# Kernel optimization log

Hardware: AMD Instinct MI355X
Metric: run time of the kernel (lower is better)

## Reference

```python
import jax, jax.numpy as jnp
import numpy as np

N_NODES = 100000
N_EDGES = 1600000
DIM = 128
N_LAYERS = 3
N_GRAPHS = 2048


def setup_inputs() -> dict:
    key = jax.random.key(0)
    ks = jax.random.split(key, 6)
    x = jax.random.normal(ks[0], (N_NODES, DIM), dtype=jnp.float32)
    edge_index = jax.random.randint(ks[1], (2, N_EDGES), 0, N_NODES, dtype=jnp.int64)
    batch = jnp.sort(jax.random.randint(ks[2], (N_NODES,), 0, N_GRAPHS, dtype=jnp.int64))
    scale = 1.0 / np.sqrt(DIM)
    W1 = jax.random.normal(ks[3], (N_LAYERS, DIM, DIM), dtype=jnp.float32) * scale
    b1 = jnp.zeros((N_LAYERS, DIM), dtype=jnp.float32)
    W2 = jax.random.normal(ks[4], (N_LAYERS, DIM, DIM), dtype=jnp.float32) * scale
    b2 = jnp.zeros((N_LAYERS, DIM), dtype=jnp.float32)
    return {"x": x, "edge_index": edge_index, "batch": batch,
            "W1": W1, "b1": b1, "W2": W2, "b2": b2}


def reference(x, edge_index, batch, W1, b1, W2, b2):
    src, dst = edge_index[0], edge_index[1]
    n = x.shape[0]
    n_layers = W1.shape[0]
    for l in range(n_layers):
        # GINConv (eps=0): h_i = MLP( sum_{j in N(i)} x_j + x_i )
        agg = jax.ops.segment_sum(x[src], dst, num_segments=n)  # [N, D]
        h = agg + x
        h = jnp.maximum(h @ W1[l] + b1[l], 0.0) @ W2[l] + b2[l]
        x = jnp.maximum(h, 0.0)  # outer self.act
    # global_mean_pool over graph ids
    sums = jax.ops.segment_sum(x, batch, num_segments=N_GRAPHS)  # [G, D]
    counts = jax.ops.segment_sum(jnp.ones((n,), x.dtype), batch, num_segments=N_GRAPHS)
    return sums / jnp.maximum(counts, 1.0)[:, None]
```

## Files before the change

### kernel.cpp

```cpp
#include <hip/hip_runtime.h>
#include <hip/hip_bf16.h>
#include <stdint.h>

#define N_NODES  100000
#define N_PAD    100032
#define N_EDGES  1600000
#define DIM      128
#define N_LAYERS 3
#define N_GRAPHS 2048

#define BSHIFT   8
#define NBUCKET  391
#define P1CHUNK  4096
#define P1GRID   391

typedef _Float16 f16;
typedef __attribute__((ext_vector_type(4))) _Float16 f16x4;
typedef __attribute__((ext_vector_type(8))) _Float16 f16x8;
typedef __attribute__((ext_vector_type(4))) float f32x4;

#define MFMA16(a, b, c) __builtin_amdgcn_mfma_f32_16x16x32_f16((a), (b), (c), 0, 0, 0)

#define OFF_OFFS  0u
#define OFF_BHT   400064u
#define OFF_BST   401664u
#define OFF_GCUR  403264u
#define OFF_BLKH  404864u
#define OFF_ESRC  1016448u
#define OFF_PAIR  7416448u
#define OFF_X16   13816448u
#define OFF_A16   39424640u
#define OFF_B16   65032832u
#define OFF_W1T   90641024u
#define OFF_W2T   90739328u


__global__ __launch_bounds__(256) void k_bhist(const int* __restrict__ dst,
                                               int* __restrict__ btot, int* __restrict__ blkh) {
    __shared__ int h[NBUCKET];
    int tid = threadIdx.x, b = blockIdx.x;
    for (int i = tid; i < NBUCKET; i += 256) h[i] = 0;
    __syncthreads();
    int base = b * P1CHUNK;
    int n = min(P1CHUNK, N_EDGES - base);
    for (int i = tid; i < n; i += 256)
        atomicAdd(&h[dst[base + i] >> BSHIFT], 1);
    __syncthreads();
    for (int i = tid; i < NBUCKET; i += 256) {
        blkh[b * NBUCKET + i] = h[i];
        atomicAdd(&btot[i], h[i]);
    }
}

__global__ __launch_bounds__(256) void k_bscan(const int* __restrict__ btot,
                                               int* __restrict__ bstart,
                                               int* __restrict__ gcursor,
                                               int* __restrict__ offs) {
    __shared__ int s[512];
    int t = threadIdx.x;
    s[t]       = (t < NBUCKET) ? btot[t] : 0;
    s[t + 256] = (t + 256 < NBUCKET) ? btot[t + 256] : 0;
    __syncthreads();
    for (int off = 1; off < 512; off <<= 1) {
        int a0 = (t >= off) ? s[t - off] : 0;
        int a1 = (t + 256 >= off) ? s[t + 256 - off] : 0;
        __syncthreads();
        s[t] += a0; s[t + 256] += a1;
        __syncthreads();
    }
    int e0 = (t == 0) ? 0 : s[t - 1];
    int e1 = s[t + 255];
    if (t < NBUCKET) { bstart[t] = e0; gcursor[t] = e0; }
    int idx = t + 256;
    if (idx <= NBUCKET) { bstart[idx] = e1; if (idx < NBUCKET) gcursor[idx] = e1; }
    if (t == 0) offs[N_NODES] = N_EDGES;
}

__global__ __launch_bounds__(256) void k_part1(const int* __restrict__ src, const int* __restrict__ dst,
                                               const int* __restrict__ blkh, int* __restrict__ gcursor,
                                               uint32_t* __restrict__ pairs) {
    __shared__ int gbase[NBUCKET];
    __shared__ int cur[NBUCKET];
    int tid = threadIdx.x, b = blockIdx.x;
    for (int i = tid; i < NBUCKET; i += 256) {
        int h = blkh[b * NBUCKET + i];
        gbase[i] = atomicAdd(&gcursor[i], h);
        cur[i] = 0;
    }
    __syncthreads();
    int base = b * P1CHUNK;
    int n = min(P1CHUNK, N_EDGES - base);
    for (int i = tid; i < n; i += 256) {
        int d = dst[base + i], s = src[base + i];
        int bin = d >> BSHIFT;
        int slot = atomicAdd(&cur[bin], 1);
        pairs[gbase[bin] + slot] = ((uint32_t)s << 8) | (uint32_t)(d & 255);
    }
}

__global__ __launch_bounds__(256) void k_part2(const uint32_t* __restrict__ pairs,
                                               const int* __restrict__ bstart,
                                               int* __restrict__ offs, int* __restrict__ esrc) {
    __shared__ int cnt[256];
    __shared__ int cur[256];
    __shared__ int sc[256];
    int t = threadIdx.x, b = blockIdx.x;
    int n0 = b << BSHIFT;
    int nn = min(256, N_NODES - n0);
    int e0 = bstart[b], e1 = bstart[b + 1];
    cnt[t] = 0;
    __syncthreads();
    for (int i = e0 + t; i < e1; i += 256)
        atomicAdd(&cnt[pairs[i] & 255], 1);
    __syncthreads();
    int my = cnt[t];
    sc[t] = my;
    __syncthreads();
    for (int off = 1; off < 256; off <<= 1) {
        int v = (t >= off) ? sc[t - off] : 0;
        __syncthreads();
        sc[t] += v;
        __syncthreads();
    }
    int excl = sc[t] - my;
    cur[t] = excl;
    if (t < nn) offs[n0 + t] = e0 + excl;
    __syncthreads();
    for (int i = e0 + t; i < e1; i += 256) {
        uint32_t p = pairs[i];
        int pos = e0 + atomicAdd(&cur[p & 255], 1);
        esrc[pos] = (int)(p >> 8);
    }
}


__global__ void k_cvtX(const float* __restrict__ x, f16* __restrict__ o) {
    size_t i = ((size_t)blockIdx.x * 256 + threadIdx.x) * 8;
    float4 v0 = *(const float4*)&x[i];
    float4 v1 = *(const float4*)&x[i + 4];
    f16x8 h;
    h[0] = (f16)v0.x; h[1] = (f16)v0.y; h[2] = (f16)v0.z; h[3] = (f16)v0.w;
    h[4] = (f16)v1.x; h[5] = (f16)v1.y; h[6] = (f16)v1.z; h[7] = (f16)v1.w;
    *(f16x8*)&o[i] = h;
}

__global__ void k_cvtW(const float* __restrict__ W1, const float* __restrict__ W2,
                       f16* __restrict__ W1t, f16* __restrict__ W2t) {
    int t = blockIdx.x * 256 + threadIdx.x;
    bool first = t < 49152;
    const float* W = first ? W1 : W2;
    f16* Wt = first ? W1t : W2t;
    int u = first ? t : t - 49152;
    int l = u >> 14;
    int kn = u & 16383;
    int k = kn >> 7, nn = kn & 127;
    Wt[l * 16384 + nn * 128 + k] = (f16)W[u];
}


#define BM 64
#define LDS_K 136

__global__ __launch_bounds__(256) void k_fused(
    const f16* __restrict__ xin, f16* __restrict__ xout,
    const int* __restrict__ offs, const int* __restrict__ esrc,
    const f16* __restrict__ W1t, const float* __restrict__ b1,
    const f16* __restrict__ W2t, const float* __restrict__ b2)
{
    __shared__ __align__(16) f16 tile[BM * LDS_K];
    int tid  = threadIdx.x;
    int lane = tid & 63;
    int w    = tid >> 6;
    int fr   = lane & 15;
    int fg   = lane >> 4;
    int row0 = blockIdx.x * BM;

    {
        const f16x8* xr = (const f16x8*)xin;
        int c = fr;
#pragma unroll
        for (int t4 = 0; t4 < 4; t4++) {
            int r = w * 16 + t4 * 4 + fg;
            int node = row0 + r;
            f16x8 sum = {(f16)0, (f16)0, (f16)0, (f16)0, (f16)0, (f16)0, (f16)0, (f16)0};
            if (node < N_NODES) {
                sum = xr[(size_t)node * 16 + c];
                int e0 = offs[node], e1 = offs[node + 1];
                int e = e0;
                for (; e + 8 <= e1; e += 8) {
                    int s0 = esrc[e + 0], s1 = esrc[e + 1], s2 = esrc[e + 2], s3 = esrc[e + 3];
                    int s4 = esrc[e + 4], s5 = esrc[e + 5], s6 = esrc[e + 6], s7 = esrc[e + 7];
                    f16x8 v0 = xr[(size_t)s0 * 16 + c], v1 = xr[(size_t)s1 * 16 + c];
                    f16x8 v2 = xr[(size_t)s2 * 16 + c], v3 = xr[(size_t)s3 * 16 + c];
                    f16x8 v4 = xr[(size_t)s4 * 16 + c], v5 = xr[(size_t)s5 * 16 + c];
                    f16x8 v6 = xr[(size_t)s6 * 16 + c], v7 = xr[(size_t)s7 * 16 + c];
                    sum += (v0 + v1) + (v2 + v3);
                    sum += (v4 + v5) + (v6 + v7);
                }
                if (e < e1) {
                    int i1 = e + 1, i2 = e + 2, i3 = e + 3, i4 = e + 4, i5 = e + 5, i6 = e + 6, i7 = e + 7;
                    bool k1 = i1 < e1, k2 = i2 < e1, k3 = i3 < e1, k4 = i4 < e1,
                         k5 = i5 < e1, k6 = i6 < e1, k7 = i7 < e1;
                    int s0 = esrc[e];
                    int s1 = esrc[k1 ? i1 : e], s2 = esrc[k2 ? i2 : e], s3 = esrc[k3 ? i3 : e];
                    int s4 = esrc[k4 ? i4 : e], s5 = esrc[k5 ? i5 : e], s6 = esrc[k6 ? i6 : e];
                    int s7 = esrc[k7 ? i7 : e];
                    f16x8 v0 = xr[(size_t)s0 * 16 + c], v1 = xr[(size_t)s1 * 16 + c];
                    f16x8 v2 = xr[(size_t)s2 * 16 + c], v3 = xr[(size_t)s3 * 16 + c];
                    f16x8 v4 = xr[(size_t)s4 * 16 + c], v5 = xr[(size_t)s5 * 16 + c];
                    f16x8 v6 = xr[(size_t)s6 * 16 + c], v7 = xr[(size_t)s7 * 16 + c];
                    sum += v0;
                    if (k1) sum += v1;
                    if (k2) sum += v2;
                    if (k3) sum += v3;
                    if (k4) sum += v4;
                    if (k5) sum += v5;
                    if (k6) sum += v6;
                    if (k7) sum += v7;
                }
            }
            *(f16x8*)&tile[r * LDS_K + c * 8] = sum;
        }
    }

    f16x8 wf[2][4];
    float4 bv[2];
#pragma unroll
    for (int nt = 0; nt < 2; nt++) {
        int col = w * 32 + nt * 16 + fr;
#pragma unroll
        for (int ks = 0; ks < 4; ks++)
            wf[nt][ks] = *(const f16x8*)&W1t[col * DIM + ks * 32 + fg * 8];
        bv[nt] = *(const float4*)&b1[w * 32 + nt * 16 + fg * 4];
    }
    __syncthreads();

    f32x4 acc[4][2];
#pragma unroll
    for (int mt = 0; mt < 4; mt++)
#pragma unroll
        for (int nt = 0; nt < 2; nt++) acc[mt][nt] = (f32x4){0.f, 0.f, 0.f, 0.f};

#pragma unroll
    for (int mt = 0; mt < 4; mt++)
#pragma unroll
        for (int ks = 0; ks < 4; ks++) {
            f16x8 a = *(const f16x8*)&tile[(mt * 16 + fr) * LDS_K + ks * 32 + fg * 8];
            acc[mt][0] = MFMA16(wf[0][ks], a, acc[mt][0]);
            acc[mt][1] = MFMA16(wf[1][ks], a, acc[mt][1]);
        }
    __syncthreads();

#pragma unroll
    for (int mt = 0; mt < 4; mt++)
#pragma unroll
        for (int nt = 0; nt < 2; nt++) {
            f16x4 hv;
            hv[0] = (f16)fmaxf(acc[mt][nt][0] + bv[nt].x, 0.f);
            hv[1] = (f16)fmaxf(acc[mt][nt][1] + bv[nt].y, 0.f);
            hv[2] = (f16)fmaxf(acc[mt][nt][2] + bv[nt].z, 0.f);
            hv[3] = (f16)fmaxf(acc[mt][nt][3] + bv[nt].w, 0.f);
            *(f16x4*)&tile[(mt * 16 + fr) * LDS_K + w * 32 + nt * 16 + fg * 4] = hv;
        }

#pragma unroll
    for (int nt = 0; nt < 2; nt++) {
        int col = w * 32 + nt * 16 + fr;
#pragma unroll
        for (int ks = 0; ks < 4; ks++)
            wf[nt][ks] = *(const f16x8*)&W2t[col * DIM + ks * 32 + fg * 8];
        bv[nt] = *(const float4*)&b2[w * 32 + nt * 16 + fg * 4];
    }
    __syncthreads();

#pragma unroll
    for (int mt = 0; mt < 4; mt++)
#pragma unroll
        for (int nt = 0; nt < 2; nt++) acc[mt][nt] = (f32x4){0.f, 0.f, 0.f, 0.f};

#pragma unroll
    for (int mt = 0; mt < 4; mt++)
#pragma unroll
        for (int ks = 0; ks < 4; ks++) {
            f16x8 a = *(const f16x8*)&tile[(mt * 16 + fr) * LDS_K + ks * 32 + fg * 8];
            acc[mt][0] = MFMA16(wf[0][ks], a, acc[mt][0]);
            acc[mt][1] = MFMA16(wf[1][ks], a, acc[mt][1]);
        }

#pragma unroll
    for (int mt = 0; mt < 4; mt++)
#pragma unroll
        for (int nt = 0; nt < 2; nt++) {
            f16x4 ov;
            ov[0] = (f16)fmaxf(acc[mt][nt][0] + bv[nt].x, 0.f);
            ov[1] = (f16)fmaxf(acc[mt][nt][1] + bv[nt].y, 0.f);
            ov[2] = (f16)fmaxf(acc[mt][nt][2] + bv[nt].z, 0.f);
            ov[3] = (f16)fmaxf(acc[mt][nt][3] + bv[nt].w, 0.f);
            *(f16x4*)&xout[(size_t)(row0 + mt * 16 + fr) * DIM + w * 32 + nt * 16 + fg * 4] = ov;
        }
}


__global__ void k_pool(const f16* __restrict__ xf, const int* __restrict__ batch,
                       float* __restrict__ out) {
    int g = blockIdx.x;
    int d = threadIdx.x;
    int lo = 0, hi = N_NODES;
    while (lo < hi) { int m = (lo + hi) >> 1; if (batch[m] < g) lo = m + 1; else hi = m; }
    int start = lo;
    hi = N_NODES;
    while (lo < hi) { int m = (lo + hi) >> 1; if (batch[m] <= g) lo = m + 1; else hi = m; }
    int end = lo;
    float acc = 0.f;
    for (int i = start; i < end; i++) acc += (float)xf[(size_t)i * DIM + d];
    float cntf = (float)(end - start);
    out[(size_t)g * DIM + d] = acc / fmaxf(cntf, 1.f);
}


extern "C" void kernel_launch(void* const* d_in, const int* in_sizes, int n_in,
                              void* d_out, int out_size, void* d_ws, size_t ws_size,
                              hipStream_t stream) {
    const float* x     = (const float*)d_in[0];
    const int*   ei    = (const int*)d_in[1];
    const int*   batch = (const int*)d_in[2];
    const float* W1    = (const float*)d_in[3];
    const float* b1    = (const float*)d_in[4];
    const float* W2    = (const float*)d_in[5];
    const float* b2    = (const float*)d_in[6];
    const int* srcp = ei;
    const int* dstp = ei + N_EDGES;

    char* ws = (char*)d_ws;
    int*      offs  = (int*)(ws + OFF_OFFS);
    int*      btot  = (int*)(ws + OFF_BHT);
    int*      bst   = (int*)(ws + OFF_BST);
    int*      gcur  = (int*)(ws + OFF_GCUR);
    int*      blkh  = (int*)(ws + OFF_BLKH);
    int*      esrc  = (int*)(ws + OFF_ESRC);
    uint32_t* pairs = (uint32_t*)(ws + OFF_PAIR);
    f16*      x16   = (f16*)(ws + OFF_X16);
    f16*      a16   = (f16*)(ws + OFF_A16);
    f16*      b16   = (f16*)(ws + OFF_B16);
    f16*      w1t   = (f16*)(ws + OFF_W1T);
    f16*      w2t   = (f16*)(ws + OFF_W2T);
    float*    outp  = (float*)d_out;

    hipMemsetAsync(btot, 0, NBUCKET * sizeof(int), stream);
    k_bhist<<<P1GRID, 256, 0, stream>>>(dstp, btot, blkh);
    k_bscan<<<1, 256, 0, stream>>>(btot, bst, gcur, offs);
    k_part1<<<P1GRID, 256, 0, stream>>>(srcp, dstp, blkh, gcur, pairs);
    k_part2<<<NBUCKET, 256, 0, stream>>>(pairs, bst, offs, esrc);

    k_cvtX<<<6250, 256, 0, stream>>>(x, x16);
    k_cvtW<<<384, 256, 0, stream>>>(W1, W2, w1t, w2t);

    const f16* xin = x16;
    for (int l = 0; l < N_LAYERS; ++l) {
        f16* xoutb = (l == 1) ? b16 : a16;
        k_fused<<<N_PAD / BM, 256, 0, stream>>>(xin, xoutb, offs, esrc,
                                                w1t + (size_t)l * DIM * DIM, b1 + (size_t)l * DIM,
                                                w2t + (size_t)l * DIM * DIM, b2 + (size_t)l * DIM);
        xin = xoutb;
    }

    k_pool<<<N_GRAPHS, 128, 0, stream>>>(xin, batch, outp);
}
```

Baseline: 322.0 us.

## Fuse mean-pool into last GIN layer, widen blocks to 512, merge convert kernels

Changes the fused layer kernel to 512 threads per block, so each wave handles 16 output columns and 2 gather rows instead of 32 columns and 4 rows. This raises parallelism for the latency-bound neighbor gather. The last layer now reduces its output tile per graph into the output through float atomics, so the final features are never written out and read back. A small division kernel then applies the node counts. The x and W conversion kernels are merged into one launch, which adds an output memset and atomic contention on graph sums that span tile boundaries.

```diff
diff --git a/kernel.cpp b/kernel.cpp
--- a/kernel.cpp
+++ b/kernel.cpp
@@ -134,40 +134,47 @@
 }
 
 
-__global__ void k_cvtX(const float* __restrict__ x, f16* __restrict__ o) {
-    size_t i = ((size_t)blockIdx.x * 256 + threadIdx.x) * 8;
-    float4 v0 = *(const float4*)&x[i];
-    float4 v1 = *(const float4*)&x[i + 4];
-    f16x8 h;
-    h[0] = (f16)v0.x; h[1] = (f16)v0.y; h[2] = (f16)v0.z; h[3] = (f16)v0.w;
-    h[4] = (f16)v1.x; h[5] = (f16)v1.y; h[6] = (f16)v1.z; h[7] = (f16)v1.w;
-    *(f16x8*)&o[i] = h;
-}
-
-__global__ void k_cvtW(const float* __restrict__ W1, const float* __restrict__ W2,
-                       f16* __restrict__ W1t, f16* __restrict__ W2t) {
-    int t = blockIdx.x * 256 + threadIdx.x;
-    bool first = t < 49152;
-    const float* W = first ? W1 : W2;
-    f16* Wt = first ? W1t : W2t;
-    int u = first ? t : t - 49152;
-    int l = u >> 14;
-    int kn = u & 16383;
-    int k = kn >> 7, nn = kn & 127;
-    Wt[l * 16384 + nn * 128 + k] = (f16)W[u];
+#define CVTX_BLOCKS 6250
+
+__global__ void k_cvt(const float* __restrict__ x,
+                      const float* __restrict__ W1, const float* __restrict__ W2,
+                      f16* __restrict__ x16, f16* __restrict__ W1t, f16* __restrict__ W2t) {
+    int b = blockIdx.x;
+    if (b < CVTX_BLOCKS) {
+        size_t i = ((size_t)b * 256 + threadIdx.x) * 8;
+        float4 v0 = *(const float4*)&x[i];
+        float4 v1 = *(const float4*)&x[i + 4];
+        f16x8 h;
+        h[0] = (f16)v0.x; h[1] = (f16)v0.y; h[2] = (f16)v0.z; h[3] = (f16)v0.w;
+        h[4] = (f16)v1.x; h[5] = (f16)v1.y; h[6] = (f16)v1.z; h[7] = (f16)v1.w;
+        *(f16x8*)&x16[i] = h;
+    } else {
+        int t = (b - CVTX_BLOCKS) * 256 + threadIdx.x;
+        bool first = t < 49152;
+        const float* W = first ? W1 : W2;
+        f16* Wt = first ? W1t : W2t;
+        int u = first ? t : t - 49152;
+        int l = u >> 14;
+        int kn = u & 16383;
+        int k = kn >> 7, nn = kn & 127;
+        Wt[l * 16384 + nn * 128 + k] = (f16)W[u];
+    }
 }
 
 
 #define BM 64
 #define LDS_K 136
 
-__global__ __launch_bounds__(256) void k_fused(
+template <bool POOL>
+__global__ __launch_bounds__(512) void k_fused(
     const f16* __restrict__ xin, f16* __restrict__ xout,
     const int* __restrict__ offs, const int* __restrict__ esrc,
     const f16* __restrict__ W1t, const float* __restrict__ b1,
-    const f16* __restrict__ W2t, const float* __restrict__ b2)
+    const f16* __restrict__ W2t, const float* __restrict__ b2,
+    const int* __restrict__ batch, float* __restrict__ gsum)
 {
     __shared__ __align__(16) f16 tile[BM * LDS_K];
+    __shared__ int sbatch[BM];
     int tid  = threadIdx.x;
     int lane = tid & 63;
     int w    = tid >> 6;
@@ -175,12 +182,17 @@
     int fg   = lane >> 4;
     int row0 = blockIdx.x * BM;
 
+    if (POOL && tid < BM) {
+        int node = row0 + tid;
+        sbatch[tid] = (node < N_NODES) ? batch[node] : -1;
+    }
+
     {
         const f16x8* xr = (const f16x8*)xin;
         int c = fr;
 #pragma unroll
-        for (int t4 = 0; t4 < 4; t4++) {
-            int r = w * 16 + t4 * 4 + fg;
+        for (int b_ = 0; b_ < 2; b_++) {
+            int r = w * 8 + b_ * 4 + fg;
             int node = row0 + r;
             f16x8 sum = {(f16)0, (f16)0, (f16)0, (f16)0, (f16)0, (f16)0, (f16)0, (f16)0};
             if (node < N_NODES) {
@@ -223,86 +235,95 @@
         }
     }
 
-    f16x8 wf[2][4];
-    float4 bv[2];
-#pragma unroll
-    for (int nt = 0; nt < 2; nt++) {
-        int col = w * 32 + nt * 16 + fr;
-#pragma unroll
-        for (int ks = 0; ks < 4; ks++)
-            wf[nt][ks] = *(const f16x8*)&W1t[col * DIM + ks * 32 + fg * 8];
-        bv[nt] = *(const float4*)&b1[w * 32 + nt * 16 + fg * 4];
-    }
-    __syncthreads();
-
-    f32x4 acc[4][2];
-#pragma unroll
-    for (int mt = 0; mt < 4; mt++)
-#pragma unroll
-        for (int nt = 0; nt < 2; nt++) acc[mt][nt] = (f32x4){0.f, 0.f, 0.f, 0.f};
-
+    int col = w * 16 + fr;
+    f16x8 wf[4];
+    float4 bv;
+#pragma unroll
+    for (int ks = 0; ks < 4; ks++)
+        wf[ks] = *(const f16x8*)&W1t[col * DIM + ks * 32 + fg * 8];
+    bv = *(const float4*)&b1[w * 16 + fg * 4];
+    __syncthreads();
+
+    f32x4 acc[4];
+#pragma unroll
+    for (int mt = 0; mt < 4; mt++) acc[mt] = (f32x4){0.f, 0.f, 0.f, 0.f};
 #pragma unroll
     for (int mt = 0; mt < 4; mt++)
 #pragma unroll
         for (int ks = 0; ks < 4; ks++) {
             f16x8 a = *(const f16x8*)&tile[(mt * 16 + fr) * LDS_K + ks * 32 + fg * 8];
-            acc[mt][0] = MFMA16(wf[0][ks], a, acc[mt][0]);
-            acc[mt][1] = MFMA16(wf[1][ks], a, acc[mt][1]);
-        }
-    __syncthreads();
-
-#pragma unroll
-    for (int mt = 0; mt < 4; mt++)
-#pragma unroll
-        for (int nt = 0; nt < 2; nt++) {
-            f16x4 hv;
-            hv[0] = (f16)fmaxf(acc[mt][nt][0] + bv[nt].x, 0.f);
-            hv[1] = (f16)fmaxf(acc[mt][nt][1] + bv[nt].y, 0.f);
-            hv[2] = (f16)fmaxf(acc[mt][nt][2] + bv[nt].z, 0.f);
-            hv[3] = (f16)fmaxf(acc[mt][nt][3] + bv[nt].w, 0.f);
-            *(f16x4*)&tile[(mt * 16 + fr) * LDS_K + w * 32 + nt * 16 + fg * 4] = hv;
-        }
-
-#pragma unroll
-    for (int nt = 0; nt < 2; nt++) {
-        int col = w * 32 + nt * 16 + fr;
-#pragma unroll
-        for (int ks = 0; ks < 4; ks++)
-            wf[nt][ks] = *(const f16x8*)&W2t[col * DIM + ks * 32 + fg * 8];
-        bv[nt] = *(const float4*)&b2[w * 32 + nt * 16 + fg * 4];
-    }
-    __syncthreads();
-
-#pragma unroll
-    for (int mt = 0; mt < 4; mt++)
-#pragma unroll
-        for (int nt = 0; nt < 2; nt++) acc[mt][nt] = (f32x4){0.f, 0.f, 0.f, 0.f};
-
+            acc[mt] = MFMA16(wf[ks], a, acc[mt]);
+        }
+    __syncthreads();
+
+#pragma unroll
+    for (int mt = 0; mt < 4; mt++) {
+        f16x4 hv;
+        hv[0] = (f16)fmaxf(acc[mt][0] + bv.x, 0.f);
+        hv[1] = (f16)fmaxf(acc[mt][1] + bv.y, 0.f);
+        hv[2] = (f16)fmaxf(acc[mt][2] + bv.z, 0.f);
+        hv[3] = (f16)fmaxf(acc[mt][3] + bv.w, 0.f);
+        *(f16x4*)&tile[(mt * 16 + fr) * LDS_K + w * 16 + fg * 4] = hv;
+    }
+
+#pragma unroll
+    for (int ks = 0; ks < 4; ks++)
+        wf[ks] = *(const f16x8*)&W2t[col * DIM + ks * 32 + fg * 8];
+    bv = *(const float4*)&b2[w * 16 + fg * 4];
+    __syncthreads();
+
+#pragma unroll
+    for (int mt = 0; mt < 4; mt++) acc[mt] = (f32x4){0.f, 0.f, 0.f, 0.f};
 #pragma unroll
     for (int mt = 0; mt < 4; mt++)
 #pragma unroll
         for (int ks = 0; ks < 4; ks++) {
             f16x8 a = *(const f16x8*)&tile[(mt * 16 + fr) * LDS_K + ks * 32 + fg * 8];
-            acc[mt][0] = MFMA16(wf[0][ks], a, acc[mt][0]);
-            acc[mt][1] = MFMA16(wf[1][ks], a, acc[mt][1]);
-        }
-
-#pragma unroll
-    for (int mt = 0; mt < 4; mt++)
-#pragma unroll
-        for (int nt = 0; nt < 2; nt++) {
+            acc[mt] = MFMA16(wf[ks], a, acc[mt]);
+        }
+
+    if (!POOL) {
+#pragma unroll
+        for (int mt = 0; mt < 4; mt++) {
             f16x4 ov;
-            ov[0] = (f16)fmaxf(acc[mt][nt][0] + bv[nt].x, 0.f);
-            ov[1] = (f16)fmaxf(acc[mt][nt][1] + bv[nt].y, 0.f);
-            ov[2] = (f16)fmaxf(acc[mt][nt][2] + bv[nt].z, 0.f);
-            ov[3] = (f16)fmaxf(acc[mt][nt][3] + bv[nt].w, 0.f);
-            *(f16x4*)&xout[(size_t)(row0 + mt * 16 + fr) * DIM + w * 32 + nt * 16 + fg * 4] = ov;
-        }
-}
-
-
-__global__ void k_pool(const f16* __restrict__ xf, const int* __restrict__ batch,
-                       float* __restrict__ out) {
+            ov[0] = (f16)fmaxf(acc[mt][0] + bv.x, 0.f);
+            ov[1] = (f16)fmaxf(acc[mt][1] + bv.y, 0.f);
+            ov[2] = (f16)fmaxf(acc[mt][2] + bv.z, 0.f);
+            ov[3] = (f16)fmaxf(acc[mt][3] + bv.w, 0.f);
+            *(f16x4*)&xout[(size_t)(row0 + mt * 16 + fr) * DIM + w * 16 + fg * 4] = ov;
+        }
+    } else {
+        __syncthreads();
+#pragma unroll
+        for (int mt = 0; mt < 4; mt++) {
+            f16x4 ov;
+            ov[0] = (f16)fmaxf(acc[mt][0] + bv.x, 0.f);
+            ov[1] = (f16)fmaxf(acc[mt][1] + bv.y, 0.f);
+            ov[2] = (f16)fmaxf(acc[mt][2] + bv.z, 0.f);
+            ov[3] = (f16)fmaxf(acc[mt][3] + bv.w, 0.f);
+            *(f16x4*)&tile[(mt * 16 + fr) * LDS_K + w * 16 + fg * 4] = ov;
+        }
+        __syncthreads();
+
+        int half = tid >> 7;
+        int d = tid & 127;
+        int rA = half * 16, rB = rA + 16;
+        float s = 0.f;
+        int curg = sbatch[rA];
+        for (int r = rA; r < rB; r++) {
+            int g = sbatch[r];
+            if (g != curg) {
+                if (curg >= 0) atomicAdd(&gsum[(size_t)curg * DIM + d], s);
+                s = 0.f; curg = g;
+            }
+            if (g >= 0) s += (float)tile[r * LDS_K + d];
+        }
+        if (curg >= 0) atomicAdd(&gsum[(size_t)curg * DIM + d], s);
+    }
+}
+
+
+__global__ void k_div(float* __restrict__ out, const int* __restrict__ batch) {
     int g = blockIdx.x;
     int d = threadIdx.x;
     int lo = 0, hi = N_NODES;
@@ -311,10 +332,8 @@
     hi = N_NODES;
     while (lo < hi) { int m = (lo + hi) >> 1; if (batch[m] <= g) lo = m + 1; else hi = m; }
     int end = lo;
-    float acc = 0.f;
-    for (int i = start; i < end; i++) acc += (float)xf[(size_t)i * DIM + d];
     float cntf = (float)(end - start);
-    out[(size_t)g * DIM + d] = acc / fmaxf(cntf, 1.f);
+    out[(size_t)g * DIM + d] /= fmaxf(cntf, 1.f);
 }
 
 
@@ -352,17 +371,16 @@
     k_part1<<<P1GRID, 256, 0, stream>>>(srcp, dstp, blkh, gcur, pairs);
     k_part2<<<NBUCKET, 256, 0, stream>>>(pairs, bst, offs, esrc);
 
-    k_cvtX<<<6250, 256, 0, stream>>>(x, x16);
-    k_cvtW<<<384, 256, 0, stream>>>(W1, W2, w1t, w2t);
-
-    const f16* xin = x16;
-    for (int l = 0; l < N_LAYERS; ++l) {
-        f16* xoutb = (l == 1) ? b16 : a16;
-        k_fused<<<N_PAD / BM, 256, 0, stream>>>(xin, xoutb, offs, esrc,
-                                                w1t + (size_t)l * DIM * DIM, b1 + (size_t)l * DIM,
-                                                w2t + (size_t)l * DIM * DIM, b2 + (size_t)l * DIM);
-        xin = xoutb;
-    }
-
-    k_pool<<<N_GRAPHS, 128, 0, stream>>>(xin, batch, outp);
-}
+    k_cvt<<<CVTX_BLOCKS + 384, 256, 0, stream>>>(x, W1, W2, x16, w1t, w2t);
+
+    hipMemsetAsync(outp, 0, (size_t)N_GRAPHS * DIM * sizeof(float), stream);
+
+    k_fused<false><<<N_PAD / BM, 512, 0, stream>>>(x16, a16, offs, esrc,
+                                                   w1t, b1, w2t, b2, batch, outp);
+    k_fused<false><<<N_PAD / BM, 512, 0, stream>>>(a16, b16, offs, esrc,
+                                                   w1t + 16384, b1 + DIM, w2t + 16384, b2 + DIM, batch, outp);
+    k_fused<true><<<N_PAD / BM, 512, 0, stream>>>(b16, a16, offs, esrc,
+                                                  w1t + 32768, b1 + 2 * DIM, w2t + 32768, b2 + 2 * DIM, batch, outp);
+
+    k_div<<<N_GRAPHS, DIM, 0, stream>>>(outp, batch);
+}
```

New measurement: 291.4 us. 9.5% less time.

## Fuse preprocessing kernels, halve fused tile rows, and fold mean-pool into last layer

Applied to the files above, without the earlier changes.

Merges x/W conversion, bucket histogram and output zeroing into a single block-dispatched preprocessing kernel, removing separate launches. The fused GIN layer kernel now processes 32 rows per block instead of 64, giving twice as many blocks for the gather-heavy aggregation. The final layer accumulates per-graph sums directly into the output via atomics, using run-length grouping of the sorted batch ids, so the last layer never writes node features and pooling does not re-read them. A small kernel then divides by counts. Atomics add nondeterministic summation order, and smaller tiles reload weights more often.

```diff
diff --git a/kernel.cpp b/kernel.cpp
--- a/kernel.cpp
+++ b/kernel.cpp
@@ -35,20 +35,56 @@
 #define OFF_W2T   90739328u
 
 
-__global__ __launch_bounds__(256) void k_bhist(const int* __restrict__ dst,
-                                               int* __restrict__ btot, int* __restrict__ blkh) {
+#define CVTX_BLOCKS 6250
+#define CVTW_BLOCKS 384
+#define ZERO_BLOCKS 128
+#define PRE_GRID    (CVTX_BLOCKS + CVTW_BLOCKS + P1GRID + ZERO_BLOCKS)
+
+__global__ __launch_bounds__(256) void k_pre(
+    const float* __restrict__ x, const float* __restrict__ W1, const float* __restrict__ W2,
+    f16* __restrict__ x16, f16* __restrict__ W1t, f16* __restrict__ W2t,
+    const int* __restrict__ dst, int* __restrict__ btot, int* __restrict__ blkh,
+    float* __restrict__ outp)
+{
     __shared__ int h[NBUCKET];
-    int tid = threadIdx.x, b = blockIdx.x;
-    for (int i = tid; i < NBUCKET; i += 256) h[i] = 0;
-    __syncthreads();
-    int base = b * P1CHUNK;
-    int n = min(P1CHUNK, N_EDGES - base);
-    for (int i = tid; i < n; i += 256)
-        atomicAdd(&h[dst[base + i] >> BSHIFT], 1);
-    __syncthreads();
-    for (int i = tid; i < NBUCKET; i += 256) {
-        blkh[b * NBUCKET + i] = h[i];
-        atomicAdd(&btot[i], h[i]);
+    int b = blockIdx.x, tid = threadIdx.x;
+    if (b < CVTX_BLOCKS) {
+        size_t i = ((size_t)b * 256 + tid) * 8;
+        float4 v0 = *(const float4*)&x[i];
+        float4 v1 = *(const float4*)&x[i + 4];
+        f16x8 o;
+        o[0] = (f16)v0.x; o[1] = (f16)v0.y; o[2] = (f16)v0.z; o[3] = (f16)v0.w;
+        o[4] = (f16)v1.x; o[5] = (f16)v1.y; o[6] = (f16)v1.z; o[7] = (f16)v1.w;
+        *(f16x8*)&x16[i] = o;
+    } else if (b < CVTX_BLOCKS + CVTW_BLOCKS) {
+        int t = (b - CVTX_BLOCKS) * 256 + tid;
+        bool first = t < 49152;
+        const float* W = first ? W1 : W2;
+        f16* Wt = first ? W1t : W2t;
+        int u = first ? t : t - 49152;
+        int l = u >> 14;
+        int kn = u & 16383;
+        int k = kn >> 7, nn = kn & 127;
+        Wt[l * 16384 + nn * 128 + k] = (f16)W[u];
+    } else if (b < CVTX_BLOCKS + CVTW_BLOCKS + P1GRID) {
+        int bb = b - CVTX_BLOCKS - CVTW_BLOCKS;
+        for (int i = tid; i < NBUCKET; i += 256) h[i] = 0;
+        __syncthreads();
+        int base = bb * P1CHUNK;
+        int n = min(P1CHUNK, N_EDGES - base);
+        for (int i = tid; i < n; i += 256)
+            atomicAdd(&h[dst[base + i] >> BSHIFT], 1);
+        __syncthreads();
+        for (int i = tid; i < NBUCKET; i += 256) {
+            blkh[bb * NBUCKET + i] = h[i];
+            atomicAdd(&btot[i], h[i]);
+        }
+    } else {
+        int bb = b - CVTX_BLOCKS - CVTW_BLOCKS - P1GRID;
+        size_t i = ((size_t)bb * 256 + tid) * 8;
+        float4 z = {0.f, 0.f, 0.f, 0.f};
+        *(float4*)&outp[i] = z;
+        *(float4*)&outp[i + 4] = z;
     }
 }
 
@@ -134,40 +170,19 @@
 }
 
 
-__global__ void k_cvtX(const float* __restrict__ x, f16* __restrict__ o) {
-    size_t i = ((size_t)blockIdx.x * 256 + threadIdx.x) * 8;
-    float4 v0 = *(const float4*)&x[i];
-    float4 v1 = *(const float4*)&x[i + 4];
-    f16x8 h;
-    h[0] = (f16)v0.x; h[1] = (f16)v0.y; h[2] = (f16)v0.z; h[3] = (f16)v0.w;
-    h[4] = (f16)v1.x; h[5] = (f16)v1.y; h[6] = (f16)v1.z; h[7] = (f16)v1.w;
-    *(f16x8*)&o[i] = h;
-}
-
-__global__ void k_cvtW(const float* __restrict__ W1, const float* __restrict__ W2,
-                       f16* __restrict__ W1t, f16* __restrict__ W2t) {
-    int t = blockIdx.x * 256 + threadIdx.x;
-    bool first = t < 49152;
-    const float* W = first ? W1 : W2;
-    f16* Wt = first ? W1t : W2t;
-    int u = first ? t : t - 49152;
-    int l = u >> 14;
-    int kn = u & 16383;
-    int k = kn >> 7, nn = kn & 127;
-    Wt[l * 16384 + nn * 128 + k] = (f16)W[u];
-}
-
-
-#define BM 64
+#define BM 32
 #define LDS_K 136
 
+template <bool POOL>
 __global__ __launch_bounds__(256) void k_fused(
     const f16* __restrict__ xin, f16* __restrict__ xout,
     const int* __restrict__ offs, const int* __restrict__ esrc,
     const f16* __restrict__ W1t, const float* __restrict__ b1,
-    const f16* __restrict__ W2t, const float* __restrict__ b2)
+    const f16* __restrict__ W2t, const float* __restrict__ b2,
+    const int* __restrict__ batch, float* __restrict__ gsum)
 {
     __shared__ __align__(16) f16 tile[BM * LDS_K];
+    __shared__ int sbatch[BM];
     int tid  = threadIdx.x;
     int lane = tid & 63;
     int w    = tid >> 6;
@@ -175,12 +190,17 @@
     int fg   = lane >> 4;
     int row0 = blockIdx.x * BM;
 
+    if (POOL && tid < BM) {
+        int node = row0 + tid;
+        sbatch[tid] = (node < N_NODES) ? batch[node] : -1;
+    }
+
     {
         const f16x8* xr = (const f16x8*)xin;
         int c = fr;
 #pragma unroll
-        for (int t4 = 0; t4 < 4; t4++) {
-            int r = w * 16 + t4 * 4 + fg;
+        for (int b_ = 0; b_ < 2; b_++) {
+            int r = w * 8 + b_ * 4 + fg;
             int node = row0 + r;
             f16x8 sum = {(f16)0, (f16)0, (f16)0, (f16)0, (f16)0, (f16)0, (f16)0, (f16)0};
             if (node < N_NODES) {
@@ -235,14 +255,14 @@
     }
     __syncthreads();
 
-    f32x4 acc[4][2];
-#pragma unroll
-    for (int mt = 0; mt < 4; mt++)
+    f32x4 acc[2][2];
+#pragma unroll
+    for (int mt = 0; mt < 2; mt++)
 #pragma unroll
         for (int nt = 0; nt < 2; nt++) acc[mt][nt] = (f32x4){0.f, 0.f, 0.f, 0.f};
 
 #pragma unroll
-    for (int mt = 0; mt < 4; mt++)
+    for (int mt = 0; mt < 2; mt++)
 #pragma unroll
         for (int ks = 0; ks < 4; ks++) {
             f16x8 a = *(const f16x8*)&tile[(mt * 16 + fr) * LDS_K + ks * 32 + fg * 8];
@@ -252,7 +272,7 @@
     __syncthreads();
 
 #pragma unroll
-    for (int mt = 0; mt < 4; mt++)
+    for (int mt = 0; mt < 2; mt++)
 #pragma unroll
         for (int nt = 0; nt < 2; nt++) {
             f16x4 hv;
@@ -274,12 +294,12 @@
     __syncthreads();
 
 #pragma unroll
-    for (int mt = 0; mt < 4; mt++)
+    for (int mt = 0; mt < 2; mt++)
 #pragma unroll
         for (int nt = 0; nt < 2; nt++) acc[mt][nt] = (f32x4){0.f, 0.f, 0.f, 0.f};
 
 #pragma unroll
-    for (int mt = 0; mt < 4; mt++)
+    for (int mt = 0; mt < 2; mt++)
 #pragma unroll
         for (int ks = 0; ks < 4; ks++) {
             f16x8 a = *(const f16x8*)&tile[(mt * 16 + fr) * LDS_K + ks * 32 + fg * 8];
@@ -287,22 +307,52 @@
             acc[mt][1] = MFMA16(wf[1][ks], a, acc[mt][1]);
         }
 
-#pragma unroll
-    for (int mt = 0; mt < 4; mt++)
-#pragma unroll
-        for (int nt = 0; nt < 2; nt++) {
-            f16x4 ov;
-            ov[0] = (f16)fmaxf(acc[mt][nt][0] + bv[nt].x, 0.f);
-            ov[1] = (f16)fmaxf(acc[mt][nt][1] + bv[nt].y, 0.f);
-            ov[2] = (f16)fmaxf(acc[mt][nt][2] + bv[nt].z, 0.f);
-            ov[3] = (f16)fmaxf(acc[mt][nt][3] + bv[nt].w, 0.f);
-            *(f16x4*)&xout[(size_t)(row0 + mt * 16 + fr) * DIM + w * 32 + nt * 16 + fg * 4] = ov;
-        }
-}
-
-
-__global__ void k_pool(const f16* __restrict__ xf, const int* __restrict__ batch,
-                       float* __restrict__ out) {
+    if (!POOL) {
+#pragma unroll
+        for (int mt = 0; mt < 2; mt++)
+#pragma unroll
+            for (int nt = 0; nt < 2; nt++) {
+                f16x4 ov;
+                ov[0] = (f16)fmaxf(acc[mt][nt][0] + bv[nt].x, 0.f);
+                ov[1] = (f16)fmaxf(acc[mt][nt][1] + bv[nt].y, 0.f);
+                ov[2] = (f16)fmaxf(acc[mt][nt][2] + bv[nt].z, 0.f);
+                ov[3] = (f16)fmaxf(acc[mt][nt][3] + bv[nt].w, 0.f);
+                *(f16x4*)&xout[(size_t)(row0 + mt * 16 + fr) * DIM + w * 32 + nt * 16 + fg * 4] = ov;
+            }
+    } else {
+        __syncthreads();
+#pragma unroll
+        for (int mt = 0; mt < 2; mt++)
+#pragma unroll
+            for (int nt = 0; nt < 2; nt++) {
+                f16x4 ov;
+                ov[0] = (f16)fmaxf(acc[mt][nt][0] + bv[nt].x, 0.f);
+                ov[1] = (f16)fmaxf(acc[mt][nt][1] + bv[nt].y, 0.f);
+                ov[2] = (f16)fmaxf(acc[mt][nt][2] + bv[nt].z, 0.f);
+                ov[3] = (f16)fmaxf(acc[mt][nt][3] + bv[nt].w, 0.f);
+                *(f16x4*)&tile[(mt * 16 + fr) * LDS_K + w * 32 + nt * 16 + fg * 4] = ov;
+            }
+        __syncthreads();
+
+        int half = tid >> 7;
+        int d = tid & 127;
+        int rA = half * 16, rB = rA + 16;
+        float s = 0.f;
+        int curg = sbatch[rA];
+        for (int r = rA; r < rB; r++) {
+            int g = sbatch[r];
+            if (g != curg) {
+                if (curg >= 0) atomicAdd(&gsum[(size_t)curg * DIM + d], s);
+                s = 0.f; curg = g;
+            }
+            if (g >= 0) s += (float)tile[r * LDS_K + d];
+        }
+        if (curg >= 0) atomicAdd(&gsum[(size_t)curg * DIM + d], s);
+    }
+}
+
+
+__global__ void k_div(float* __restrict__ out, const int* __restrict__ batch) {
     int g = blockIdx.x;
     int d = threadIdx.x;
     int lo = 0, hi = N_NODES;
@@ -311,10 +361,8 @@
     hi = N_NODES;
     while (lo < hi) { int m = (lo + hi) >> 1; if (batch[m] <= g) lo = m + 1; else hi = m; }
     int end = lo;
-    float acc = 0.f;
-    for (int i = start; i < end; i++) acc += (float)xf[(size_t)i * DIM + d];
     float cntf = (float)(end - start);
-    out[(size_t)g * DIM + d] = acc / fmaxf(cntf, 1.f);
+    out[(size_t)g * DIM + d] /= fmaxf(cntf, 1.f);
 }
 
 
@@ -347,22 +395,18 @@
     float*    outp  = (float*)d_out;
 
     hipMemsetAsync(btot, 0, NBUCKET * sizeof(int), stream);
-    k_bhist<<<P1GRID, 256, 0, stream>>>(dstp, btot, blkh);
+    k_pre<<<PRE_GRID, 256, 0, stream>>>(x, W1, W2, x16, w1t, w2t, dstp, btot, blkh, outp);
+
     k_bscan<<<1, 256, 0, stream>>>(btot, bst, gcur, offs);
     k_part1<<<P1GRID, 256, 0, stream>>>(srcp, dstp, blkh, gcur, pairs);
     k_part2<<<NBUCKET, 256, 0, stream>>>(pairs, bst, offs, esrc);
 
-    k_cvtX<<<6250, 256, 0, stream>>>(x, x16);
-    k_cvtW<<<384, 256, 0, stream>>>(W1, W2, w1t, w2t);
-
-    const f16* xin = x16;
-    for (int l = 0; l < N_LAYERS; ++l) {
-        f16* xoutb = (l == 1) ? b16 : a16;
-        k_fused<<<N_PAD / BM, 256, 0, stream>>>(xin, xoutb, offs, esrc,
-                                                w1t + (size_t)l * DIM * DIM, b1 + (size_t)l * DIM,
-                                                w2t + (size_t)l * DIM * DIM, b2 + (size_t)l * DIM);
-        xin = xoutb;
-    }
-
-    k_pool<<<N_GRAPHS, 128, 0, stream>>>(xin, batch, outp);
-}
+    k_fused<false><<<N_PAD / BM, 256, 0, stream>>>(x16, a16, offs, esrc,
+                                                   w1t, b1, w2t, b2, batch, outp);
+    k_fused<false><<<N_PAD / BM, 256, 0, stream>>>(a16, b16, offs, esrc,
+                                                   w1t + 16384, b1 + DIM, w2t + 16384, b2 + DIM, batch, outp);
+    k_fused<true><<<N_PAD / BM, 256, 0, stream>>>(b16, a16, offs, esrc,
+                                                  w1t + 32768, b1 + 2 * DIM, w2t + 32768, b2 + 2 * DIM, batch, outp);
+
+    k_div<<<N_GRAPHS, DIM, 0, stream>>>(outp, batch);
+}
```

After: 302.4 us. -6.1%, faster.
